# Kernel optimization log

Hardware: AMD Instinct MI355X
Metric: run time of the kernel (lower is better)

Reference implementation:

```python
import jax, jax.numpy as jnp
import numpy as np

N_NODES = 100000
N_EDGES = 1600000
D_FEAT = 64


def setup_inputs() -> dict:
    key = jax.random.key(0)
    k1, k2, k3 = jax.random.split(key, 3)
    features = jax.random.normal(k1, (N_NODES, D_FEAT), dtype=jnp.float32)
    neigh_idx = jax.random.randint(k2, (N_EDGES,), 0, N_NODES, dtype=jnp.int64)
    # sorted segment ids: each destination node's neighbor edges are contiguous
    seg_ids = jnp.sort(jax.random.randint(k3, (N_EDGES,), 0, N_NODES, dtype=jnp.int64))
    return {"features": features, "neigh_idx": neigh_idx, "seg_ids": seg_ids}


def reference(features, neigh_idx, seg_ids):
    # Aggregator with pooling_type='sum', gcn=False, num_sample=None.
    # Original: dense one-hot mask [B, U] @ features[unique] == sum of neighbor
    # feature rows per batch node == gather + segment-sum over the edge list.
    gathered = features[neigh_idx]  # [E, d]
    to_feats = jax.ops.segment_sum(
        gathered, seg_ids, num_segments=features.shape[0], indices_are_sorted=True
    )  # [N, d]
    return to_feats
```

## Files before the change

### kernel.cpp

```cpp
#include <hip/hip_runtime.h>
#include <hip/hip_bf16.h>

#define N_NODES 100000
#define N_EDGES 1600000
#define D_FEAT  64

#define OFF_WS_BYTES   ((((N_NODES + 1) * 4) + 1023) & ~1023)
#define BF16_WS_BYTES  ((size_t)N_NODES * D_FEAT * 2)
#define OFFSET_BLOCKS  ((N_NODES + 1 + 255) / 256)
#define CONVERT_BLOCKS 2048

__global__ __launch_bounds__(256) void prep_kernel(
        const float* __restrict__ feat,
        const int* __restrict__ seg_ids,
        int* __restrict__ offsets,
        ushort* __restrict__ fb) {
    int b = blockIdx.x;
    if (b < OFFSET_BLOCKS) {
        int n = b * 256 + threadIdx.x;
        if (n > N_NODES) return;
        int lo = 0, hi = N_EDGES;
        while (lo < hi) {
            int mid = (lo + hi) >> 1;
            if (seg_ids[mid] < n) lo = mid + 1; else hi = mid;
        }
        offsets[n] = lo;
    } else {
        const int total = N_NODES * D_FEAT / 4;
        int tid = (b - OFFSET_BLOCKS) * 256 + threadIdx.x;
        for (int i = tid; i < total; i += CONVERT_BLOCKS * 256) {
            float4 v = reinterpret_cast<const float4*>(feat)[i];
            uint ux = __float_as_uint(v.x), uy = __float_as_uint(v.y);
            uint uz = __float_as_uint(v.z), uw = __float_as_uint(v.w);
            ushort4 o;
            o.x = (ushort)((ux + 0x7fffu + ((ux >> 16) & 1u)) >> 16);
            o.y = (ushort)((uy + 0x7fffu + ((uy >> 16) & 1u)) >> 16);
            o.z = (ushort)((uz + 0x7fffu + ((uz >> 16) & 1u)) >> 16);
            o.w = (ushort)((uw + 0x7fffu + ((uw >> 16) & 1u)) >> 16);
            reinterpret_cast<ushort4*>(fb)[i] = o;
        }
    }
}

__global__ __launch_bounds__(256) void aggregate_bf16_kernel(
        const ushort* __restrict__ fb,
        const int* __restrict__ neigh_idx,
        const int* __restrict__ offsets,
        float* __restrict__ out) {
    int node = blockIdx.x * 4 + (threadIdx.x >> 6);
    if (node >= N_NODES) return;
    int lane = threadIdx.x & 63;
    int slot = lane >> 3;
    int ch   = lane & 7;

    int s = offsets[node];
    int e = offsets[node + 1];

    float a0[8], a1[8];
    #pragma unroll
    for (int k = 0; k < 8; ++k) { a0[k] = 0.f; a1[k] = 0.f; }

    for (int cb = s; cb < e; cb += 64) {
        int li = cb + lane;
        int ci = (li < e) ? li : (e - 1);
        int my_idx = neigh_idx[ci];
        int lim = e - cb; if (lim > 64) lim = 64;

        for (int p = 0; p < lim; p += 16) {
            int p0 = p + slot, p1 = p0 + 8;
            int q0 = (p0 < lim) ? p0 : (lim - 1);
            int q1 = (p1 < lim) ? p1 : (lim - 1);
            float m0 = (p0 < lim) ? 1.f : 0.f;
            float m1 = (p1 < lim) ? 1.f : 0.f;
            int n0 = __shfl(my_idx, q0);
            int n1 = __shfl(my_idx, q1);
            uint4 w0 = reinterpret_cast<const uint4*>(fb + (size_t)n0 * D_FEAT)[ch];
            uint4 w1 = reinterpret_cast<const uint4*>(fb + (size_t)n1 * D_FEAT)[ch];
            a0[0] = fmaf(m0, __uint_as_float(w0.x << 16),         a0[0]);
            a0[1] = fmaf(m0, __uint_as_float(w0.x & 0xFFFF0000u), a0[1]);
            a0[2] = fmaf(m0, __uint_as_float(w0.y << 16),         a0[2]);
            a0[3] = fmaf(m0, __uint_as_float(w0.y & 0xFFFF0000u), a0[3]);
            a0[4] = fmaf(m0, __uint_as_float(w0.z << 16),         a0[4]);
            a0[5] = fmaf(m0, __uint_as_float(w0.z & 0xFFFF0000u), a0[5]);
            a0[6] = fmaf(m0, __uint_as_float(w0.w << 16),         a0[6]);
            a0[7] = fmaf(m0, __uint_as_float(w0.w & 0xFFFF0000u), a0[7]);
            a1[0] = fmaf(m1, __uint_as_float(w1.x << 16),         a1[0]);
            a1[1] = fmaf(m1, __uint_as_float(w1.x & 0xFFFF0000u), a1[1]);
            a1[2] = fmaf(m1, __uint_as_float(w1.y << 16),         a1[2]);
            a1[3] = fmaf(m1, __uint_as_float(w1.y & 0xFFFF0000u), a1[3]);
            a1[4] = fmaf(m1, __uint_as_float(w1.z << 16),         a1[4]);
            a1[5] = fmaf(m1, __uint_as_float(w1.z & 0xFFFF0000u), a1[5]);
            a1[6] = fmaf(m1, __uint_as_float(w1.w << 16),         a1[6]);
            a1[7] = fmaf(m1, __uint_as_float(w1.w & 0xFFFF0000u), a1[7]);
        }
    }

    float r[8];
    #pragma unroll
    for (int k = 0; k < 8; ++k) r[k] = a0[k] + a1[k];
    #pragma unroll
    for (int k = 0; k < 8; ++k) {
        r[k] += __shfl_xor(r[k], 8);
        r[k] += __shfl_xor(r[k], 16);
        r[k] += __shfl_xor(r[k], 32);
    }

    if (lane < 8) {
        float4* orow = reinterpret_cast<float4*>(out + (size_t)node * D_FEAT);
        orow[2 * ch]     = make_float4(r[0], r[1], r[2], r[3]);
        orow[2 * ch + 1] = make_float4(r[4], r[5], r[6], r[7]);
    }
}

__global__ __launch_bounds__(256) void aggregate_kernel(
        const float* __restrict__ feat,
        const int* __restrict__ neigh_idx,
        const int* __restrict__ offsets,
        float* __restrict__ out) {
    int node  = blockIdx.x * 4 + (threadIdx.x >> 6);
    if (node >= N_NODES) return;
    int lane  = threadIdx.x & 63;
    int sub   = lane >> 4;
    int chunk = lane & 15;

    int s = offsets[node];
    int e = offsets[node + 1];

    float4 a0 = make_float4(0.f, 0.f, 0.f, 0.f);
    float4 a1 = make_float4(0.f, 0.f, 0.f, 0.f);

    for (int base = s; base < e; base += 8) {
        int i0 = base + sub, i1 = i0 + 4;
        int c0 = (i0 < e) ? i0 : (e - 1);
        int c1 = (i1 < e) ? i1 : (e - 1);
        float m0 = (i0 < e) ? 1.f : 0.f;
        float m1 = (i1 < e) ? 1.f : 0.f;
        int n0 = neigh_idx[c0], n1 = neigh_idx[c1];
        float4 v0 = reinterpret_cast<const float4*>(feat + (size_t)n0 * D_FEAT)[chunk];
        float4 v1 = reinterpret_cast<const float4*>(feat + (size_t)n1 * D_FEAT)[chunk];
        a0.x = fmaf(m0, v0.x, a0.x); a0.y = fmaf(m0, v0.y, a0.y);
        a0.z = fmaf(m0, v0.z, a0.z); a0.w = fmaf(m0, v0.w, a0.w);
        a1.x = fmaf(m1, v1.x, a1.x); a1.y = fmaf(m1, v1.y, a1.y);
        a1.z = fmaf(m1, v1.z, a1.z); a1.w = fmaf(m1, v1.w, a1.w);
    }

    float4 acc;
    acc.x = a0.x + a1.x; acc.y = a0.y + a1.y;
    acc.z = a0.z + a1.z; acc.w = a0.w + a1.w;
    acc.x += __shfl_xor(acc.x, 16); acc.y += __shfl_xor(acc.y, 16);
    acc.z += __shfl_xor(acc.z, 16); acc.w += __shfl_xor(acc.w, 16);
    acc.x += __shfl_xor(acc.x, 32); acc.y += __shfl_xor(acc.y, 32);
    acc.z += __shfl_xor(acc.z, 32); acc.w += __shfl_xor(acc.w, 32);

    if (lane < 16) {
        reinterpret_cast<float4*>(out + (size_t)node * D_FEAT)[chunk] = acc;
    }
}

extern "C" void kernel_launch(void* const* d_in, const int* in_sizes, int n_in,
                              void* d_out, int out_size, void* d_ws, size_t ws_size,
                              hipStream_t stream) {
    const float* features  = (const float*)d_in[0];
    const int*   neigh_idx = (const int*)d_in[1];
    const int*   seg_ids   = (const int*)d_in[2];
    float*       out       = (float*)d_out;
    int*         offsets   = (int*)d_ws;

    bool bf16_path = (ws_size >= (size_t)OFF_WS_BYTES + BF16_WS_BYTES);
    if (bf16_path) {
        ushort* fb = (ushort*)((char*)d_ws + OFF_WS_BYTES);
        prep_kernel<<<OFFSET_BLOCKS + CONVERT_BLOCKS, 256, 0, stream>>>(
            features, seg_ids, offsets, fb);
        int grid = (N_NODES + 3) / 4;
        aggregate_bf16_kernel<<<grid, 256, 0, stream>>>(fb, neigh_idx, offsets, out);
    } else {
        int total = N_NODES + 1;
        int grid1 = (total + 255) / 256;
        prep_kernel<<<grid1 < OFFSET_BLOCKS ? grid1 : OFFSET_BLOCKS, 256, 0, stream>>>(
            features, seg_ids, offsets, (ushort*)nullptr);
        int grid = (N_NODES + 3) / 4;
        aggregate_kernel<<<grid, 256, 0, stream>>>(features, neigh_idx, offsets, out);
    }
}
```

Before: 51.61 us.

## Switch to edge-parallel segmented reduction with boundary fixup kernel

Replaces the node-per-wavefront aggregation with an edge-window approach where each wavefront processes a fixed 64-edge window. Runs are reduced within lanes and then across slots through shared memory. Segments crossing window boundaries go to head/tail workspace buffers, and a cleanup kernel merges them and zero-fills empty nodes. This is meant to remove load imbalance and per-node loop overhead from variable segment lengths. The cost is an extra kernel launch, extra workspace traffic, and a path that only runs if the workspace is large enough.

```diff
diff --git a/kernel.cpp b/kernel.cpp
--- a/kernel.cpp
+++ b/kernel.cpp
@@ -4,9 +4,11 @@
 #define N_NODES 100000
 #define N_EDGES 1600000
 #define D_FEAT  64
+#define NWIN    (N_EDGES / 64)
 
 #define OFF_WS_BYTES   ((((N_NODES + 1) * 4) + 1023) & ~1023)
 #define BF16_WS_BYTES  ((size_t)N_NODES * D_FEAT * 2)
+#define HW_WS_BYTES    ((size_t)NWIN * D_FEAT * 4)
 #define OFFSET_BLOCKS  ((N_NODES + 1 + 255) / 256)
 #define CONVERT_BLOCKS 2048
 
@@ -42,6 +44,176 @@
     }
 }
 
+__device__ __forceinline__ void unpack8(uint4 u, float* f) {
+    f[0] = __uint_as_float(u.x << 16);
+    f[1] = __uint_as_float(u.x & 0xFFFF0000u);
+    f[2] = __uint_as_float(u.y << 16);
+    f[3] = __uint_as_float(u.y & 0xFFFF0000u);
+    f[4] = __uint_as_float(u.z << 16);
+    f[5] = __uint_as_float(u.z & 0xFFFF0000u);
+    f[6] = __uint_as_float(u.w << 16);
+    f[7] = __uint_as_float(u.w & 0xFFFF0000u);
+}
+
+__global__ __launch_bounds__(256) void aggregate_seg_kernel(
+        const ushort* __restrict__ fb,
+        const int* __restrict__ neigh_idx,
+        const int* __restrict__ seg_ids,
+        float* __restrict__ out,
+        float* __restrict__ hw,
+        float* __restrict__ tw) {
+    __shared__ float s_val[4][16][64];
+    __shared__ int   s_seg[4][16];
+    __shared__ int   s_valid[4][16];
+
+    int wid  = threadIdx.x >> 6;
+    int w    = blockIdx.x * 4 + wid;
+    int lane = threadIdx.x & 63;
+    int slot = lane >> 3;
+    int ch   = lane & 7;
+    int base = w * 64;
+
+    int my_idx = neigh_idx[base + lane];
+    int my_seg = seg_ids[base + lane];
+    int seg_prev = (w > 0)        ? seg_ids[base - 1]  : -1;
+    int seg_next = (w < NWIN - 1) ? seg_ids[base + 64] : -1;
+
+    int e0 = slot * 8;
+    int n0 = __shfl(my_idx, e0 + 0);
+    int n1 = __shfl(my_idx, e0 + 1);
+    int n2 = __shfl(my_idx, e0 + 2);
+    int n3 = __shfl(my_idx, e0 + 3);
+    int n4 = __shfl(my_idx, e0 + 4);
+    int n5 = __shfl(my_idx, e0 + 5);
+    int n6 = __shfl(my_idx, e0 + 6);
+    int n7 = __shfl(my_idx, e0 + 7);
+
+    const uint4* tb = reinterpret_cast<const uint4*>(fb);
+    uint4 w0 = tb[(size_t)n0 * 8 + ch];
+    uint4 w1 = tb[(size_t)n1 * 8 + ch];
+    uint4 w2 = tb[(size_t)n2 * 8 + ch];
+    uint4 w3 = tb[(size_t)n3 * 8 + ch];
+    uint4 w4 = tb[(size_t)n4 * 8 + ch];
+    uint4 w5 = tb[(size_t)n5 * 8 + ch];
+    uint4 w6 = tb[(size_t)n6 * 8 + ch];
+    uint4 w7 = tb[(size_t)n7 * 8 + ch];
+
+    int sg0 = __shfl(my_seg, e0 + 0);
+    int sg1 = __shfl(my_seg, e0 + 1);
+    int sg2 = __shfl(my_seg, e0 + 2);
+    int sg3 = __shfl(my_seg, e0 + 3);
+    int sg4 = __shfl(my_seg, e0 + 4);
+    int sg5 = __shfl(my_seg, e0 + 5);
+    int sg6 = __shfl(my_seg, e0 + 6);
+    int sg7 = __shfl(my_seg, e0 + 7);
+
+    float acc[8], Hs[8], t_[8];
+    int curseg, runstart, hseg = -1;
+    unpack8(w0, acc);
+    curseg = sg0; runstart = 0;
+
+#define STEP(WL, SGL, LNUM)                                                   \
+    if (SGL == curseg) {                                                      \
+        unpack8(WL, t_);                                                      \
+        _Pragma("unroll") for (int j = 0; j < 8; ++j) acc[j] += t_[j];        \
+    } else {                                                                  \
+        if (runstart == 0) {                                                  \
+            hseg = curseg;                                                    \
+            _Pragma("unroll") for (int j = 0; j < 8; ++j) Hs[j] = acc[j];     \
+        } else {                                                              \
+            float4* orow = reinterpret_cast<float4*>(out + (size_t)curseg * 64); \
+            orow[ch * 2]     = make_float4(acc[0], acc[1], acc[2], acc[3]);   \
+            orow[ch * 2 + 1] = make_float4(acc[4], acc[5], acc[6], acc[7]);   \
+        }                                                                     \
+        unpack8(WL, acc); curseg = SGL; runstart = LNUM;                      \
+    }
+
+    STEP(w1, sg1, 1)
+    STEP(w2, sg2, 2)
+    STEP(w3, sg3, 3)
+    STEP(w4, sg4, 4)
+    STEP(w5, sg5, 5)
+    STEP(w6, sg6, 6)
+    STEP(w7, sg7, 7)
+#undef STEP
+
+    float* item0 = &s_val[wid][2 * slot][0];
+    float* item1 = &s_val[wid][2 * slot + 1][0];
+    if (runstart == 0) {
+        reinterpret_cast<float4*>(item0)[ch * 2]     = make_float4(acc[0], acc[1], acc[2], acc[3]);
+        reinterpret_cast<float4*>(item0)[ch * 2 + 1] = make_float4(acc[4], acc[5], acc[6], acc[7]);
+        if (ch == 0) {
+            s_seg[wid][2 * slot] = curseg;
+            s_valid[wid][2 * slot] = 1;
+            s_valid[wid][2 * slot + 1] = 0;
+        }
+    } else {
+        reinterpret_cast<float4*>(item0)[ch * 2]     = make_float4(Hs[0], Hs[1], Hs[2], Hs[3]);
+        reinterpret_cast<float4*>(item0)[ch * 2 + 1] = make_float4(Hs[4], Hs[5], Hs[6], Hs[7]);
+        reinterpret_cast<float4*>(item1)[ch * 2]     = make_float4(acc[0], acc[1], acc[2], acc[3]);
+        reinterpret_cast<float4*>(item1)[ch * 2 + 1] = make_float4(acc[4], acc[5], acc[6], acc[7]);
+        if (ch == 0) {
+            s_seg[wid][2 * slot] = hseg;
+            s_seg[wid][2 * slot + 1] = curseg;
+            s_valid[wid][2 * slot] = 1;
+            s_valid[wid][2 * slot + 1] = 1;
+        }
+    }
+    __syncthreads();
+
+    int mseg = -1, startItem = -1;
+    float macc = 0.f;
+#define EMIT(SEG, VAL, TSTART, TEND)                                          \
+    {                                                                         \
+        if ((TSTART) && (SEG) == seg_prev)                                    \
+            hw[(size_t)w * 64 + lane] = (VAL);                                \
+        else if ((TEND) && (SEG) == seg_next)                                 \
+            tw[(size_t)w * 64 + lane] = (VAL);                                \
+        else                                                                  \
+            out[(size_t)(SEG) * 64 + lane] = (VAL);                          \
+    }
+    for (int i = 0; i < 16; ++i) {
+        if (!s_valid[wid][i]) continue;
+        int sgi = s_seg[wid][i];
+        float v = s_val[wid][i][lane];
+        if (mseg < 0) { mseg = sgi; macc = v; startItem = i; }
+        else if (sgi == mseg) { macc += v; }
+        else {
+            EMIT(mseg, macc, startItem == 0, false)
+            mseg = sgi; macc = v; startItem = i;
+        }
+    }
+    EMIT(mseg, macc, startItem == 0, true)
+#undef EMIT
+}
+
+#define BOUNDARY_BLOCKS ((NWIN - 1 + 3) / 4)
+__global__ __launch_bounds__(256) void cleanup_kernel(
+        const int* __restrict__ seg_ids,
+        const int* __restrict__ offsets,
+        const float* __restrict__ hw,
+        const float* __restrict__ tw,
+        float* __restrict__ out) {
+    if (blockIdx.x < BOUNDARY_BLOCKS) {
+        int b = blockIdx.x * 4 + (threadIdx.x >> 6) + 1;
+        if (b >= NWIN) return;
+        int lane = threadIdx.x & 63;
+        int sL = seg_ids[b * 64 - 1];
+        int sR = seg_ids[b * 64];
+        if (sL == sR)
+            out[(size_t)sR * 64 + lane] =
+                tw[(size_t)(b - 1) * 64 + lane] + hw[(size_t)b * 64 + lane];
+    } else {
+        int n = (blockIdx.x - BOUNDARY_BLOCKS) * 256 + threadIdx.x;
+        if (n < N_NODES && offsets[n] == offsets[n + 1]) {
+            float4 z = make_float4(0.f, 0.f, 0.f, 0.f);
+            float4* orow = reinterpret_cast<float4*>(out + (size_t)n * 64);
+            #pragma unroll
+            for (int k = 0; k < 16; ++k) orow[k] = z;
+        }
+    }
+}
+
 __global__ __launch_bounds__(256) void aggregate_bf16_kernel(
         const ushort* __restrict__ fb,
         const int* __restrict__ neigh_idx,
@@ -52,20 +224,16 @@
     int lane = threadIdx.x & 63;
     int slot = lane >> 3;
     int ch   = lane & 7;
-
     int s = offsets[node];
     int e = offsets[node + 1];
-
     float a0[8], a1[8];
     #pragma unroll
     for (int k = 0; k < 8; ++k) { a0[k] = 0.f; a1[k] = 0.f; }
-
     for (int cb = s; cb < e; cb += 64) {
         int li = cb + lane;
         int ci = (li < e) ? li : (e - 1);
         int my_idx = neigh_idx[ci];
         int lim = e - cb; if (lim > 64) lim = 64;
-
         for (int p = 0; p < lim; p += 16) {
             int p0 = p + slot, p1 = p0 + 8;
             int q0 = (p0 < lim) ? p0 : (lim - 1);
@@ -76,25 +244,12 @@
             int n1 = __shfl(my_idx, q1);
             uint4 w0 = reinterpret_cast<const uint4*>(fb + (size_t)n0 * D_FEAT)[ch];
             uint4 w1 = reinterpret_cast<const uint4*>(fb + (size_t)n1 * D_FEAT)[ch];
-            a0[0] = fmaf(m0, __uint_as_float(w0.x << 16),         a0[0]);
-            a0[1] = fmaf(m0, __uint_as_float(w0.x & 0xFFFF0000u), a0[1]);
-            a0[2] = fmaf(m0, __uint_as_float(w0.y << 16),         a0[2]);
-            a0[3] = fmaf(m0, __uint_as_float(w0.y & 0xFFFF0000u), a0[3]);
-            a0[4] = fmaf(m0, __uint_as_float(w0.z << 16),         a0[4]);
-            a0[5] = fmaf(m0, __uint_as_float(w0.z & 0xFFFF0000u), a0[5]);
-            a0[6] = fmaf(m0, __uint_as_float(w0.w << 16),         a0[6]);
-            a0[7] = fmaf(m0, __uint_as_float(w0.w & 0xFFFF0000u), a0[7]);
-            a1[0] = fmaf(m1, __uint_as_float(w1.x << 16),         a1[0]);
-            a1[1] = fmaf(m1, __uint_as_float(w1.x & 0xFFFF0000u), a1[1]);
-            a1[2] = fmaf(m1, __uint_as_float(w1.y << 16),         a1[2]);
-            a1[3] = fmaf(m1, __uint_as_float(w1.y & 0xFFFF0000u), a1[3]);
-            a1[4] = fmaf(m1, __uint_as_float(w1.z << 16),         a1[4]);
-            a1[5] = fmaf(m1, __uint_as_float(w1.z & 0xFFFF0000u), a1[5]);
-            a1[6] = fmaf(m1, __uint_as_float(w1.w << 16),         a1[6]);
-            a1[7] = fmaf(m1, __uint_as_float(w1.w & 0xFFFF0000u), a1[7]);
-        }
-    }
-
+            float f0[8], f1[8];
+            unpack8(w0, f0); unpack8(w1, f1);
+            #pragma unroll
+            for (int j = 0; j < 8; ++j) { a0[j] = fmaf(m0, f0[j], a0[j]); a1[j] = fmaf(m1, f1[j], a1[j]); }
+        }
+    }
     float r[8];
     #pragma unroll
     for (int k = 0; k < 8; ++k) r[k] = a0[k] + a1[k];
@@ -104,7 +259,6 @@
         r[k] += __shfl_xor(r[k], 16);
         r[k] += __shfl_xor(r[k], 32);
     }
-
     if (lane < 8) {
         float4* orow = reinterpret_cast<float4*>(out + (size_t)node * D_FEAT);
         orow[2 * ch]     = make_float4(r[0], r[1], r[2], r[3]);
@@ -112,7 +266,7 @@
     }
 }
 
-__global__ __launch_bounds__(256) void aggregate_kernel(
+__global__ __launch_bounds__(256) void aggregate_f32_kernel(
         const float* __restrict__ feat,
         const int* __restrict__ neigh_idx,
         const int* __restrict__ offsets,
@@ -122,13 +276,10 @@
     int lane  = threadIdx.x & 63;
     int sub   = lane >> 4;
     int chunk = lane & 15;
-
     int s = offsets[node];
     int e = offsets[node + 1];
-
     float4 a0 = make_float4(0.f, 0.f, 0.f, 0.f);
     float4 a1 = make_float4(0.f, 0.f, 0.f, 0.f);
-
     for (int base = s; base < e; base += 8) {
         int i0 = base + sub, i1 = i0 + 4;
         int c0 = (i0 < e) ? i0 : (e - 1);
@@ -143,7 +294,6 @@
         a1.x = fmaf(m1, v1.x, a1.x); a1.y = fmaf(m1, v1.y, a1.y);
         a1.z = fmaf(m1, v1.z, a1.z); a1.w = fmaf(m1, v1.w, a1.w);
     }
-
     float4 acc;
     acc.x = a0.x + a1.x; acc.y = a0.y + a1.y;
     acc.z = a0.z + a1.z; acc.w = a0.w + a1.w;
@@ -151,7 +301,6 @@
     acc.z += __shfl_xor(acc.z, 16); acc.w += __shfl_xor(acc.w, 16);
     acc.x += __shfl_xor(acc.x, 32); acc.y += __shfl_xor(acc.y, 32);
     acc.z += __shfl_xor(acc.z, 32); acc.w += __shfl_xor(acc.w, 32);
-
     if (lane < 16) {
         reinterpret_cast<float4*>(out + (size_t)node * D_FEAT)[chunk] = acc;
     }
@@ -164,21 +313,32 @@
     const int*   neigh_idx = (const int*)d_in[1];
     const int*   seg_ids   = (const int*)d_in[2];
     float*       out       = (float*)d_out;
-    int*         offsets   = (int*)d_ws;
-
-    bool bf16_path = (ws_size >= (size_t)OFF_WS_BYTES + BF16_WS_BYTES);
-    if (bf16_path) {
-        ushort* fb = (ushort*)((char*)d_ws + OFF_WS_BYTES);
+    char*        wsb       = (char*)d_ws;
+    int*         offsets   = (int*)wsb;
+
+    size_t need_seg  = (size_t)OFF_WS_BYTES + BF16_WS_BYTES + 2 * HW_WS_BYTES;
+    size_t need_bf16 = (size_t)OFF_WS_BYTES + BF16_WS_BYTES;
+
+    if (ws_size >= need_seg) {
+        ushort* fb = (ushort*)(wsb + OFF_WS_BYTES);
+        float*  hw = (float*)(wsb + OFF_WS_BYTES + BF16_WS_BYTES);
+        float*  tw = hw + (size_t)NWIN * D_FEAT;
         prep_kernel<<<OFFSET_BLOCKS + CONVERT_BLOCKS, 256, 0, stream>>>(
             features, seg_ids, offsets, fb);
-        int grid = (N_NODES + 3) / 4;
-        aggregate_bf16_kernel<<<grid, 256, 0, stream>>>(fb, neigh_idx, offsets, out);
+        aggregate_seg_kernel<<<NWIN / 4, 256, 0, stream>>>(
+            fb, neigh_idx, seg_ids, out, hw, tw);
+        cleanup_kernel<<<BOUNDARY_BLOCKS + (N_NODES + 255) / 256, 256, 0, stream>>>(
+            seg_ids, offsets, hw, tw, out);
+    } else if (ws_size >= need_bf16) {
+        ushort* fb = (ushort*)(wsb + OFF_WS_BYTES);
+        prep_kernel<<<OFFSET_BLOCKS + CONVERT_BLOCKS, 256, 0, stream>>>(
+            features, seg_ids, offsets, fb);
+        aggregate_bf16_kernel<<<(N_NODES + 3) / 4, 256, 0, stream>>>(
+            fb, neigh_idx, offsets, out);
     } else {
-        int total = N_NODES + 1;
-        int grid1 = (total + 255) / 256;
-        prep_kernel<<<grid1 < OFFSET_BLOCKS ? grid1 : OFFSET_BLOCKS, 256, 0, stream>>>(
+        prep_kernel<<<OFFSET_BLOCKS, 256, 0, stream>>>(
             features, seg_ids, offsets, (ushort*)nullptr);
-        int grid = (N_NODES + 3) / 4;
-        aggregate_kernel<<<grid, 256, 0, stream>>>(features, neigh_idx, offsets, out);
-    }
-}
+        aggregate_f32_kernel<<<(N_NODES + 3) / 4, 256, 0, stream>>>(
+            features, neigh_idx, offsets, out);
+    }
+}
```

Result: slower. 53.47 us (+3.6%).
